# Optimization experiments

Measured on AMD Instinct MI355X. Metric: run time of the kernel, lower is better.

Reference implementation:

```python
import jax, jax.numpy as jnp
import numpy as np
import math

N_EMBD = 1024
NUM_HEADS = 16
HEAD_DIM = N_EMBD // NUM_HEADS


def alibi_slopes(num_heads):
    x = (2 ** 8) ** (1.0 / num_heads)
    return jnp.array([1.0 / x ** (i + 1) for i in range(num_heads)], dtype=jnp.float32)


def setup_inputs() -> dict:
    key = jax.random.key(0)
    k1, k2 = jax.random.split(key)
    x = jax.random.normal(k1, (2, 2048, N_EMBD), dtype=jnp.float32)
    W_kqv = jax.random.normal(k2, (3 * N_EMBD, N_EMBD), dtype=jnp.float32) * (1.0 / math.sqrt(N_EMBD))
    return {"x": x, "W_kqv": W_kqv}


def reference(x, W_kqv):
    B, S, E = x.shape
    H, D = NUM_HEADS, HEAD_DIM
    kqv = jnp.einsum('bse,fe->bsf', x, W_kqv)  # Linear without bias
    k, q, v = jnp.split(kqv, 3, axis=-1)       # chunk order: key, query, value
    # [B, H, S, D]
    q = q.reshape(B, S, H, D).transpose(0, 2, 1, 3)
    k = k.reshape(B, S, H, D).transpose(0, 2, 1, 3)
    v = v.reshape(B, S, H, D).transpose(0, 2, 1, 3)
    # ALiBi bias: slopes[h] * (j - i), shape [H, S, S]
    rel = jnp.arange(S)[None, :] - jnp.arange(S)[:, None]  # [S, S]
    bias = alibi_slopes(H)[:, None, None] * rel.astype(jnp.float32)
    scale = math.sqrt(E)  # NOTE: module scales by sqrt(n_embd), not sqrt(head_dim)
    score = jnp.einsum('bhqd,bhkd->bhqk', q, k) / scale + bias[None]
    causal = jnp.tril(jnp.ones((S, S), dtype=bool))
    score = jnp.where(causal[None, None], score, -jnp.inf)
    attn = jax.nn.softmax(score, axis=-1)
    out = jnp.einsum('bhqk,bhkd->bhqd', attn, v)
    return out.transpose(0, 2, 1, 3).reshape(B, S, E)
```

## Files before the change

### kernel.cpp

```cpp
#include <hip/hip_runtime.h>
#include <hip/hip_bf16.h>
#include <math.h>

#define TOTAL_B 2
#define SEQ 2048
#define EMB 1024
#define NH 16
#define HD 64
#define M_GEMM (TOTAL_B*SEQ)
#define N_GEMM (3*EMB)
#define K_GEMM EMB

typedef __attribute__((ext_vector_type(8))) short short8;
typedef __attribute__((ext_vector_type(4))) float f32x4;
typedef __attribute__((ext_vector_type(4))) unsigned u32x4;

static __device__ __forceinline__ short f2bf(float f) {
  union { float f; unsigned u; } v; v.f = f;
  unsigned r = v.u + 0x7fff + ((v.u >> 16) & 1u);
  return (short)(r >> 16);
}

static __device__ __forceinline__ void gload_lds16(const void* g, void* l) {
  __builtin_amdgcn_global_load_lds(
      (const __attribute__((address_space(1))) void*)(uintptr_t)g,
      (__attribute__((address_space(3))) void*)(uintptr_t)l, 16, 0, 0);
}

static __device__ __forceinline__ float exp2v(float x) {
  float r; asm("v_exp_f32 %0, %1" : "=v"(r) : "v"(x)); return r;
}
static __device__ __forceinline__ unsigned cvtpk(float lo, float hi) {
  unsigned r; asm("v_cvt_pk_bf16_f32 %0, %1, %2" : "=v"(r) : "v"(lo), "v"(hi)); return r;
}
static __device__ __forceinline__ void pl32swap(unsigned &a, unsigned &b) {
  asm("v_permlane32_swap_b32 %0, %1" : "+v"(a), "+v"(b));
}

__global__ void cvt_kernel(const float* __restrict__ x, const float* __restrict__ w,
                           short* __restrict__ xb, short* __restrict__ wb) {
  const long nx = (long)M_GEMM * K_GEMM;
  const long nw = (long)N_GEMM * K_GEMM;
  long i = (long)blockIdx.x * blockDim.x + threadIdx.x;
  const long tot = (nx + nw) / 8;
  if (i >= tot) return;
  long e = i * 8;
  const float* s; short* d;
  if (e < nx) { s = x + e; d = xb + e; }
  else        { s = w + (e - nx); d = wb + (e - nx); }
  float4 a = ((const float4*)s)[0];
  float4 b = ((const float4*)s)[1];
  short8 o;
  o[0]=f2bf(a.x); o[1]=f2bf(a.y); o[2]=f2bf(a.z); o[3]=f2bf(a.w);
  o[4]=f2bf(b.x); o[5]=f2bf(b.y); o[6]=f2bf(b.z); o[7]=f2bf(b.w);
  *(short8*)d = o;
}

__global__ __launch_bounds__(512, 2) void qkv_gemm(const short* __restrict__ A, const short* __restrict__ Bm,
                                                   short* __restrict__ Kb, short* __restrict__ Qb,
                                                   short* __restrict__ Vb) {
  __shared__ __align__(16) short lds[57344];
  const int tid = threadIdx.x;
  const int lane = tid & 63;
  const int wid = tid >> 6;
  const int lr = lane & 15, lg = lane >> 4;
  const int m0 = blockIdx.y * 256, n0 = blockIdx.x * 192;
  const int wr = wid >> 1;
  const int wc = wid & 1;
  const int srcRow = tid >> 3;
  const int srcCh  = (tid & 7) ^ (srcRow & 7);

  f32x4 acc[4][6] = {};

  auto stageA = [&](int buf, int kt, int u) {
    const int row = u*64 + srcRow;
    gload_lds16(A + (size_t)(m0 + row)*K_GEMM + kt*64 + srcCh*8,
                &lds[buf*16384 + u*4096 + tid*8]);
  };
  auto stageB = [&](int buf, int kt, int u) {
    const int row = u*64 + srcRow;
    gload_lds16(Bm + (size_t)(n0 + row)*K_GEMM + kt*64 + srcCh*8,
                &lds[32768 + buf*12288 + u*4096 + tid*8]);
  };
  auto readA = [&](int buf, int mi, int kk) -> short8 {
    const int r = wr*64 + mi*16 + lr;
    const int c = (kk*4 + lg) ^ (r & 7);
    return *(const short8*)(&lds[buf*16384 + r*64 + c*8]);
  };
  auto readB = [&](int buf, int nj, int kk) -> short8 {
    const int r = wc*96 + nj*16 + lr;
    const int c = (kk*4 + lg) ^ (r & 7);
    return *(const short8*)(&lds[32768 + buf*12288 + r*64 + c*8]);
  };

#pragma unroll
  for (int u = 0; u < 4; ++u) stageA(0, 0, u);
#pragma unroll
  for (int u = 0; u < 3; ++u) stageB(0, 0, u);
  asm volatile("s_waitcnt vmcnt(0)" ::: "memory");
  __builtin_amdgcn_s_barrier();

  short8 aq[2][2], bq[6][2];
  const int NT = K_GEMM / 64;
#pragma unroll 1
  for (int kt = 0; kt < NT; ++kt) {
    const int buf = kt & 1, nb = buf ^ 1;
    const bool more = (kt + 1 < NT);

#pragma unroll
    for (int kk = 0; kk < 2; ++kk) {
      aq[0][kk] = readA(buf, 0, kk); aq[1][kk] = readA(buf, 1, kk);
      bq[0][kk] = readB(buf, 0, kk); bq[1][kk] = readB(buf, 1, kk); bq[2][kk] = readB(buf, 2, kk);
    }
    if (more) { stageA(nb, kt+1, 0); stageA(nb, kt+1, 1); }
    __builtin_amdgcn_s_barrier();
    asm volatile("s_waitcnt lgkmcnt(0)" ::: "memory");
    __builtin_amdgcn_sched_barrier(0);
    __builtin_amdgcn_s_setprio(1);
#pragma unroll
    for (int mi = 0; mi < 2; ++mi)
#pragma unroll
      for (int nj = 0; nj < 3; ++nj)
#pragma unroll
        for (int kk = 0; kk < 2; ++kk)
          acc[mi][nj] = __builtin_amdgcn_mfma_f32_16x16x32_bf16(aq[mi][kk], bq[nj][kk], acc[mi][nj], 0, 0, 0);
    __builtin_amdgcn_s_setprio(0);
    __builtin_amdgcn_sched_barrier(0);
    __builtin_amdgcn_s_barrier();

#pragma unroll
    for (int kk = 0; kk < 2; ++kk) {
      bq[3][kk] = readB(buf, 3, kk); bq[4][kk] = readB(buf, 4, kk); bq[5][kk] = readB(buf, 5, kk);
    }
    if (more) { stageA(nb, kt+1, 2); stageA(nb, kt+1, 3); }
    __builtin_amdgcn_s_barrier();
    asm volatile("s_waitcnt lgkmcnt(0)" ::: "memory");
    __builtin_amdgcn_sched_barrier(0);
    __builtin_amdgcn_s_setprio(1);
#pragma unroll
    for (int mi = 0; mi < 2; ++mi)
#pragma unroll
      for (int nj = 3; nj < 6; ++nj)
#pragma unroll
        for (int kk = 0; kk < 2; ++kk)
          acc[mi][nj] = __builtin_amdgcn_mfma_f32_16x16x32_bf16(aq[mi][kk], bq[nj][kk], acc[mi][nj], 0, 0, 0);
    __builtin_amdgcn_s_setprio(0);
    __builtin_amdgcn_sched_barrier(0);
    __builtin_amdgcn_s_barrier();

#pragma unroll
    for (int kk = 0; kk < 2; ++kk) {
      aq[0][kk] = readA(buf, 2, kk); aq[1][kk] = readA(buf, 3, kk);
    }
    if (more) { stageB(nb, kt+1, 0); stageB(nb, kt+1, 1); }
    __builtin_amdgcn_s_barrier();
    asm volatile("s_waitcnt lgkmcnt(0)" ::: "memory");
    __builtin_amdgcn_sched_barrier(0);
    __builtin_amdgcn_s_setprio(1);
#pragma unroll
    for (int mi = 0; mi < 2; ++mi)
#pragma unroll
      for (int nj = 3; nj < 6; ++nj)
#pragma unroll
        for (int kk = 0; kk < 2; ++kk)
          acc[mi+2][nj] = __builtin_amdgcn_mfma_f32_16x16x32_bf16(aq[mi][kk], bq[nj][kk], acc[mi+2][nj], 0, 0, 0);
    __builtin_amdgcn_s_setprio(0);
    __builtin_amdgcn_sched_barrier(0);
    __builtin_amdgcn_s_barrier();

#pragma unroll
    for (int kk = 0; kk < 2; ++kk) {
      bq[0][kk] = readB(buf, 0, kk); bq[1][kk] = readB(buf, 1, kk); bq[2][kk] = readB(buf, 2, kk);
    }
    if (more) { stageB(nb, kt+1, 2); }
    __builtin_amdgcn_s_barrier();
    asm volatile("s_waitcnt lgkmcnt(0)" ::: "memory");
    __builtin_amdgcn_sched_barrier(0);
    __builtin_amdgcn_s_setprio(1);
#pragma unroll
    for (int mi = 0; mi < 2; ++mi)
#pragma unroll
      for (int nj = 0; nj < 3; ++nj)
#pragma unroll
        for (int kk = 0; kk < 2; ++kk)
          acc[mi+2][nj] = __builtin_amdgcn_mfma_f32_16x16x32_bf16(aq[mi][kk], bq[nj][kk], acc[mi+2][nj], 0, 0, 0);
    __builtin_amdgcn_s_setprio(0);
    __builtin_amdgcn_sched_barrier(0);

    asm volatile("s_waitcnt vmcnt(0)" ::: "memory");
    __builtin_amdgcn_s_barrier();
  }

#pragma unroll
  for (int nj = 0; nj < 6; ++nj) {
    const int f = n0 + wc*96 + nj*16 + lr;
    const int which = f >> 10, fl = f & 1023;
    const int h = fl >> 6, d = fl & 63;
    short* dst = (which == 0) ? Kb : (which == 1) ? Qb : Vb;
    const float scale = (which == 1) ? 0.04508422f : 1.0f;
    short* base = dst + (size_t)h*SEQ*HD + d;
#pragma unroll
    for (int mi = 0; mi < 4; ++mi)
#pragma unroll
      for (int r = 0; r < 4; ++r) {
        const int m = m0 + wr*64 + mi*16 + lg*4 + r;
        const int b = m >> 11, s = m & 2047;
        base[((size_t)b*NH*SEQ + s)*HD] = f2bf(acc[mi][nj][r] * scale);
      }
  }
}

__global__ void vtrans(const short* __restrict__ Vb, short* __restrict__ Vt) {
  __shared__ short t[64][72];
  const int hb = blockIdx.y;
  const int s0 = blockIdx.x * 64;
  const short* src = Vb + ((size_t)hb*SEQ + s0)*HD;
  short* dst = Vt + (size_t)hb*HD*SEQ;
  const int tid = threadIdx.x;
#pragma unroll
  for (int i = 0; i < 2; ++i) {
    const int e = i*2048 + tid*8;
    const int r = e >> 6, c = e & 63;
    short8 v = *(const short8*)(src + (size_t)r*HD + c);
#pragma unroll
    for (int j = 0; j < 8; ++j) t[r][c+j] = v[j];
  }
  __syncthreads();
#pragma unroll
  for (int i = 0; i < 2; ++i) {
    const int e = i*2048 + tid*8;
    const int d = e >> 6, ss = e & 63;
    short8 v;
#pragma unroll
    for (int j = 0; j < 8; ++j) v[j] = t[ss+j][d];
    *(short8*)(dst + (size_t)d*SEQ + s0 + ss) = v;
  }
}

__global__ __launch_bounds__(256, 4) void attn_kernel(const short* __restrict__ Kb, const short* __restrict__ Qb,
                                                      const short* __restrict__ Vt, float* __restrict__ Out) {
  __shared__ __align__(16) short Ks[2][64*64];
  __shared__ __align__(16) short Vs[2][64*64];
  const int tid = threadIdx.x, lane = tid & 63, wid = tid >> 6;
  const int lr = lane & 15, lg = lane >> 4;
  const int bh = blockIdx.x;
  const int b = bh >> 4, h = bh & 15;
  const int y = blockIdx.y;
  const int qt = (y < 8)  ? 2*y
               : (y < 16) ? 31 - 2*(y - 8)
               : (y < 24) ? 30 - 2*(y - 16)
               :            2*(y - 24) + 1;
  const float slope = exp2f(-0.5f * (float)(h + 1)) * 1.44269504f;
  const short* Kp = Kb + (size_t)bh * SEQ * HD;
  const short* Qp = Qb + (size_t)bh * SEQ * HD;
  const short* Vp = Vt + (size_t)bh * HD * SEQ;
  float* Ob = Out + (size_t)b * SEQ * EMB + (size_t)h * HD;

  const int q0 = qt * 64, qrb = q0 + wid * 16;
  const int nt = qt + 1;

  short8 qf[2];
#pragma unroll
  for (int kk = 0; kk < 2; ++kk)
    qf[kk] = *(const short8*)(Qp + (size_t)(qrb + lr)*HD + kk*32 + lg*8);

  const int bp = ((lr & 4) << 1) | ((lr & 2) << 1) | ((lr & 8) >> 2) | (lr & 1);
  const int cbase = qrb + lr - ((lg & 1) * 8 + (lg >> 1) * 2);

  float m_run = -INFINITY, l_run = 0.f;
  f32x4 o[4] = {};

  auto stageK = [&](int buf, int t) {
    const int kv0 = t * 64;
#pragma unroll
    for (int ii = 0; ii < 2; ++ii) {
      const int e16 = ii*256 + tid;
      const int row = e16 >> 3, ch = e16 & 7;
      const int sch = ch ^ (row & 7);
      gload_lds16(Kp + (size_t)(kv0 + row)*HD + sch*8, &Ks[buf][ii*2048 + wid*512]);
    }
  };
  auto stageV = [&](int buf, int t) {
    const int kv0 = t * 64;
#pragma unroll
    for (int ii = 0; ii < 2; ++ii) {
      const int e16 = ii*256 + tid;
      const int row = e16 >> 3, ch = e16 & 7;
      const int sch = ch ^ (row & 7);
      gload_lds16(Vp + (size_t)row*SEQ + kv0 + sch*8, &Vs[buf][ii*2048 + wid*512]);
    }
  };
  auto qkt = [&](int buf, f32x4* sc) {
    short8 kf[4][2];
#pragma unroll
    for (int kvf = 0; kvf < 4; ++kvf) {
      const int row = kvf*16 + bp;
#pragma unroll
      for (int kk = 0; kk < 2; ++kk) {
        const int c = (kk*4 + lg) ^ (row & 7);
        kf[kvf][kk] = *(const short8*)(&Ks[buf][row*64 + c*8]);
      }
    }
    __builtin_amdgcn_s_setprio(1);
#pragma unroll
    for (int kvf = 0; kvf < 4; ++kvf) {
      f32x4 s = {};
      s = __builtin_amdgcn_mfma_f32_16x16x32_bf16(kf[kvf][0], qf[0], s, 0, 0, 0);
      s = __builtin_amdgcn_mfma_f32_16x16x32_bf16(kf[kvf][1], qf[1], s, 0, 0, 0);
      sc[kvf] = s;
    }
    __builtin_amdgcn_s_setprio(0);
  };
  auto biasmax = [&](int tt, const f32x4* sc, float vv[4][4]) -> float {
    const float dbase = (float)(tt*64 - cbase);
    if (tt == nt - 1) {
#pragma unroll
      for (int kvf = 0; kvf < 4; ++kvf)
#pragma unroll
        for (int r = 0; r < 4; ++r) {
          const float C = (float)(kvf*16 + (r>>1)*4 + (r&1));
          const float toff = dbase + C;
          float val = fmaf(slope, toff, sc[kvf][r]);
          if (toff > 0.f) val = -INFINITY;
          vv[kvf][r] = val;
        }
    } else {
#pragma unroll
      for (int kvf = 0; kvf < 4; ++kvf)
#pragma unroll
        for (int r = 0; r < 4; ++r) {
          const float C = (float)(kvf*16 + (r>>1)*4 + (r&1));
          vv[kvf][r] = fmaf(slope, dbase + C, sc[kvf][r]);
        }
    }
    float a0 = fmaxf(fmaxf(vv[0][0], vv[0][1]), fmaxf(vv[0][2], vv[0][3]));
    float a1 = fmaxf(fmaxf(vv[1][0], vv[1][1]), fmaxf(vv[1][2], vv[1][3]));
    float a2 = fmaxf(fmaxf(vv[2][0], vv[2][1]), fmaxf(vv[2][2], vv[2][3]));
    float a3 = fmaxf(fmaxf(vv[3][0], vv[3][1]), fmaxf(vv[3][2], vv[3][3]));
    float mt = fmaxf(fmaxf(a0, a1), fmaxf(a2, a3));
    mt = fmaxf(mt, __shfl_xor(mt, 16, 64));
    mt = fmaxf(mt, __shfl_xor(mt, 32, 64));
    return mt;
  };

  stageK(0, 0);
  if (nt > 1) stageK(1, 1);
  stageV(0, 0);
  __syncthreads();
  f32x4 sc[4];
  qkt(0, sc);
  float vc[4][4];
  m_run = biasmax(0, sc, vc);
  __syncthreads();

#pragma unroll 1
  for (int t = 0; t < nt; ++t) {
    if (t + 1 < nt) stageV((t + 1) & 1, t + 1);
    if (t + 2 < nt) stageK(t & 1, t + 2);

    float vn[4][4];
    const bool have_next = (t + 1 < nt);
    if (have_next) {
      qkt((t + 1) & 1, sc);
      const float mtn = biasmax(t + 1, sc, vn);
      if (__any(mtn > m_run + 10.f)) {
        const float mn = fmaxf(m_run, mtn);
        const float corr = exp2v(m_run - mn);
        m_run = mn;
        l_run *= corr;
        float co[4];
#pragma unroll
        for (int r = 0; r < 4; ++r) co[r] = __shfl(corr, lg*4 + r, 64);
#pragma unroll
        for (int dt = 0; dt < 4; ++dt)
#pragma unroll
          for (int r = 0; r < 4; ++r) o[dt][r] *= co[r];
      }
    }

#pragma unroll
    for (int kvf = 0; kvf < 4; ++kvf)
#pragma unroll
      for (int r = 0; r < 4; ++r)
        vc[kvf][r] = exp2v(vc[kvf][r] - m_run);
    float s0 = (vc[0][0]+vc[0][1]) + (vc[0][2]+vc[0][3]);
    float s1 = (vc[1][0]+vc[1][1]) + (vc[1][2]+vc[1][3]);
    float s2 = (vc[2][0]+vc[2][1]) + (vc[2][2]+vc[2][3]);
    float s3 = (vc[3][0]+vc[3][1]) + (vc[3][2]+vc[3][3]);
    float lt = (s0+s1) + (s2+s3);
    lt += __shfl_xor(lt, 16, 64);
    lt += __shfl_xor(lt, 32, 64);
    l_run += lt;

    unsigned pk[4][2];
#pragma unroll
    for (int kvf = 0; kvf < 4; ++kvf) {
      pk[kvf][0] = cvtpk(vc[kvf][0], vc[kvf][1]);
      pk[kvf][1] = cvtpk(vc[kvf][2], vc[kvf][3]);
    }
    __builtin_amdgcn_s_setprio(1);
#pragma unroll
    for (int ks = 0; ks < 2; ++ks) {
      unsigned w0 = pk[2*ks][0], w1 = pk[2*ks+1][0];
      pl32swap(w0, w1);
      unsigned w2 = pk[2*ks][1], w3 = pk[2*ks+1][1];
      pl32swap(w2, w3);
      u32x4 wv = {w0, w1, w2, w3};
      const short8 pf = __builtin_bit_cast(short8, wv);
#pragma unroll
      for (int dt = 0; dt < 4; ++dt) {
        const int rv = dt*16 + lr;
        const int cv = (ks*4 + lg) ^ (rv & 7);
        const short8 vf = *(const short8*)(&Vs[t & 1][rv*64 + cv*8]);
        o[dt] = __builtin_amdgcn_mfma_f32_16x16x32_bf16(pf, vf, o[dt], 0, 0, 0);
      }
    }
    __builtin_amdgcn_s_setprio(0);

    __syncthreads();
    if (have_next) {
#pragma unroll
      for (int kvf = 0; kvf < 4; ++kvf)
#pragma unroll
        for (int r = 0; r < 4; ++r)
          vc[kvf][r] = vn[kvf][r];
    }
  }

  const float inv = 1.f / l_run;
  float li[4];
#pragma unroll
  for (int r = 0; r < 4; ++r) li[r] = __shfl(inv, lg*4 + r, 64);
#pragma unroll
  for (int dt = 0; dt < 4; ++dt)
#pragma unroll
    for (int r = 0; r < 4; ++r) {
      const int iq = qrb + lg*4 + r;
      Ob[(size_t)iq*EMB + dt*16 + lr] = o[dt][r] * li[r];
    }
}

extern "C" void kernel_launch(void* const* d_in, const int* in_sizes, int n_in,
                              void* d_out, int out_size, void* d_ws, size_t ws_size,
                              hipStream_t stream) {
  const float* x = (const float*)d_in[0];
  const float* w = (const float*)d_in[1];
  char* ws = (char*)d_ws;
  if (ws_size < 39845888u) return;
  short* xb = (short*)(ws);
  short* wb = (short*)(ws + 8388608u);
  short* Kb = (short*)(ws + 14680064u);
  short* Qb = (short*)(ws + 23068672u);
  short* Vb = (short*)(ws + 31457280u);
  short* Vt = xb;
  float* out = (float*)d_out;

  cvt_kernel<<<3584, 256, 0, stream>>>(x, w, xb, wb);
  qkv_gemm<<<dim3(N_GEMM/192, M_GEMM/256), 512, 0, stream>>>(xb, wb, Kb, Qb, Vb);
  vtrans<<<dim3(SEQ/64, TOTAL_B*NH), 256, 0, stream>>>(Vb, Vt);
  attn_kernel<<<dim3(TOTAL_B*NH, 32), 256, 0, stream>>>(Kb, Qb, Vt, out);
}
```

Measured before the change: 96.42 us.

## Split KV range for long causal query tiles and merge with combine kernel

```diff
diff --git a/kernel.cpp b/kernel.cpp
--- a/kernel.cpp
+++ b/kernel.cpp
@@ -238,7 +238,8 @@
 }
 
 __global__ __launch_bounds__(256, 4) void attn_kernel(const short* __restrict__ Kb, const short* __restrict__ Qb,
-                                                      const short* __restrict__ Vt, float* __restrict__ Out) {
+                                                      const short* __restrict__ Vt, float* __restrict__ Out,
+                                                      float* __restrict__ Po, float2* __restrict__ Ml) {
   __shared__ __align__(16) short Ks[2][64*64];
   __shared__ __align__(16) short Vs[2][64*64];
   const int tid = threadIdx.x, lane = tid & 63, wid = tid >> 6;
@@ -246,10 +247,16 @@
   const int bh = blockIdx.x;
   const int b = bh >> 4, h = bh & 15;
   const int y = blockIdx.y;
-  const int qt = (y < 8)  ? 2*y
-               : (y < 16) ? 31 - 2*(y - 8)
-               : (y < 24) ? 30 - 2*(y - 16)
-               :            2*(y - 24) + 1;
+  int qt, t0, t1, part;
+  if (y < 16) { qt = y; t0 = 0; t1 = qt + 1; part = -1; }
+  else {
+    const int p = (y - 16) >> 1;
+    part = (y - 16) & 1;
+    qt = 16 + p;
+    const int hh = (qt + 1) >> 1;
+    t0 = part ? hh : 0;
+    t1 = part ? qt + 1 : hh;
+  }
   const float slope = exp2f(-0.5f * (float)(h + 1)) * 1.44269504f;
   const short* Kp = Kb + (size_t)bh * SEQ * HD;
   const short* Qp = Qb + (size_t)bh * SEQ * HD;
@@ -257,7 +264,6 @@
   float* Ob = Out + (size_t)b * SEQ * EMB + (size_t)h * HD;
 
   const int q0 = qt * 64, qrb = q0 + wid * 16;
-  const int nt = qt + 1;
 
   short8 qf[2];
 #pragma unroll
@@ -313,7 +319,7 @@
   };
   auto biasmax = [&](int tt, const f32x4* sc, float vv[4][4]) -> float {
     const float dbase = (float)(tt*64 - cbase);
-    if (tt == nt - 1) {
+    if (tt == qt) {
 #pragma unroll
       for (int kvf = 0; kvf < 4; ++kvf)
 #pragma unroll
@@ -343,25 +349,26 @@
     return mt;
   };
 
-  stageK(0, 0);
-  if (nt > 1) stageK(1, 1);
-  stageV(0, 0);
+  stageK(0, t0);
+  if (t1 - t0 > 1) stageK(1, t0 + 1);
+  stageV(0, t0);
   __syncthreads();
   f32x4 sc[4];
   qkt(0, sc);
   float vc[4][4];
-  m_run = biasmax(0, sc, vc);
+  m_run = biasmax(t0, sc, vc);
   __syncthreads();
 
 #pragma unroll 1
-  for (int t = 0; t < nt; ++t) {
-    if (t + 1 < nt) stageV((t + 1) & 1, t + 1);
-    if (t + 2 < nt) stageK(t & 1, t + 2);
+  for (int t = t0; t < t1; ++t) {
+    const int u = t - t0;
+    if (t + 1 < t1) stageV((u + 1) & 1, t + 1);
+    if (t + 2 < t1) stageK(u & 1, t + 2);
 
     float vn[4][4];
-    const bool have_next = (t + 1 < nt);
+    const bool have_next = (t + 1 < t1);
     if (have_next) {
-      qkt((t + 1) & 1, sc);
+      qkt((u + 1) & 1, sc);
       const float mtn = biasmax(t + 1, sc, vn);
       if (__any(mtn > m_run + 10.f)) {
         const float mn = fmaxf(m_run, mtn);
@@ -411,7 +418,7 @@
       for (int dt = 0; dt < 4; ++dt) {
         const int rv = dt*16 + lr;
         const int cv = (ks*4 + lg) ^ (rv & 7);
-        const short8 vf = *(const short8*)(&Vs[t & 1][rv*64 + cv*8]);
+        const short8 vf = *(const short8*)(&Vs[u & 1][rv*64 + cv*8]);
         o[dt] = __builtin_amdgcn_mfma_f32_16x16x32_bf16(pf, vf, o[dt], 0, 0, 0);
       }
     }
@@ -427,17 +434,72 @@
     }
   }
 
-  const float inv = 1.f / l_run;
-  float li[4];
-#pragma unroll
-  for (int r = 0; r < 4; ++r) li[r] = __shfl(inv, lg*4 + r, 64);
-#pragma unroll
-  for (int dt = 0; dt < 4; ++dt)
-#pragma unroll
-    for (int r = 0; r < 4; ++r) {
-      const int iq = qrb + lg*4 + r;
-      Ob[(size_t)iq*EMB + dt*16 + lr] = o[dt][r] * li[r];
-    }
+  if (part < 0) {
+    const float inv = 1.f / l_run;
+    float li[4];
+#pragma unroll
+    for (int r = 0; r < 4; ++r) li[r] = __shfl(inv, lg*4 + r, 64);
+#pragma unroll
+    for (int dt = 0; dt < 4; ++dt)
+#pragma unroll
+      for (int r = 0; r < 4; ++r) {
+        const int iq = qrb + lg*4 + r;
+        Ob[(size_t)iq*EMB + dt*16 + lr] = o[dt][r] * li[r];
+      }
+  } else {
+    const int pidx = bh * 16 + (qt - 16);
+    if (lg == 0) Ml[(size_t)(pidx*2 + part)*64 + wid*16 + lr] = make_float2(m_run, l_run);
+    if (part == 0) {
+#pragma unroll
+      for (int dt = 0; dt < 4; ++dt)
+#pragma unroll
+        for (int r = 0; r < 4; ++r) {
+          const int iq = qrb + lg*4 + r;
+          Ob[(size_t)iq*EMB + dt*16 + lr] = o[dt][r];
+        }
+    } else {
+      float* pp = Po + (size_t)pidx*4096;
+#pragma unroll
+      for (int dt = 0; dt < 4; ++dt)
+#pragma unroll
+        for (int r = 0; r < 4; ++r) {
+          const int ql = wid*16 + lg*4 + r;
+          pp[ql*64 + dt*16 + lr] = o[dt][r];
+        }
+    }
+  }
+}
+
+__global__ __launch_bounds__(256) void combine_kernel(const float* __restrict__ Po, const float2* __restrict__ Ml,
+                                                      float* __restrict__ Out) {
+  const int qi = blockIdx.x;
+  const int bh = blockIdx.y;
+  const int pidx = bh*16 + qi;
+  const int qt = 16 + qi;
+  const int b = bh >> 4, h = bh & 15;
+  const int tid = threadIdx.x;
+  const int row = tid >> 2;
+  const int c0 = (tid & 3) * 16;
+  const float2 ml0 = Ml[(size_t)(pidx*2 + 0)*64 + row];
+  const float2 ml1 = Ml[(size_t)(pidx*2 + 1)*64 + row];
+  const float m = fmaxf(ml0.x, ml1.x);
+  const float e0 = exp2f(ml0.x - m), e1 = exp2f(ml1.x - m);
+  const float l = ml0.y*e0 + ml1.y*e1;
+  const float sc0 = e0 / l, sc1 = e1 / l;
+  const int q = qt*64 + row;
+  float* op = Out + (size_t)b*SEQ*EMB + (size_t)q*EMB + h*HD + c0;
+  const float* pp = Po + (size_t)pidx*4096 + row*64 + c0;
+#pragma unroll
+  for (int i = 0; i < 4; ++i) {
+    float4 a = ((const float4*)op)[i];
+    float4 c = ((const float4*)pp)[i];
+    float4 r;
+    r.x = a.x*sc0 + c.x*sc1;
+    r.y = a.y*sc0 + c.y*sc1;
+    r.z = a.z*sc0 + c.z*sc1;
+    r.w = a.w*sc0 + c.w*sc1;
+    ((float4*)op)[i] = r;
+  }
 }
 
 extern "C" void kernel_launch(void* const* d_in, const int* in_sizes, int n_in,
@@ -453,10 +515,13 @@
   short* Qb = (short*)(ws + 23068672u);
   short* Vb = (short*)(ws + 31457280u);
   short* Vt = xb;
+  float2* Ml = (float2*)(ws + 8388608u);
+  float*  Po = (float*)(ws + 31457280u);
   float* out = (float*)d_out;
 
   cvt_kernel<<<3584, 256, 0, stream>>>(x, w, xb, wb);
   qkv_gemm<<<dim3(N_GEMM/192, M_GEMM/256), 512, 0, stream>>>(xb, wb, Kb, Qb, Vb);
   vtrans<<<dim3(SEQ/64, TOTAL_B*NH), 256, 0, stream>>>(Vb, Vt);
-  attn_kernel<<<dim3(TOTAL_B*NH, 32), 256, 0, stream>>>(Kb, Qb, Vt, out);
-}
+  attn_kernel<<<dim3(TOTAL_B*NH, 48), 256, 0, stream>>>(Kb, Qb, Vt, out, Po, Ml);
+  combine_kernel<<<dim3(16, TOTAL_B*NH), 256, 0, stream>>>(Po, Ml, out);
+}
```

New measurement: 102.2 us. 6.0% more time.
